# Performance work log

Measured on AMD Instinct MI355X. Metric: run time of the kernel, lower is better.

## Reference

```python
import jax, jax.numpy as jnp
import numpy as np

B, L, HID, NH = 8, 384, 512, 8
DH = HID // NH
MAX_SEQ_LEN = 384  # module's max_seq_len; pe has 2*MAX_SEQ_LEN rows


def setup_inputs() -> dict:
    key = jax.random.key(0)
    ks = jax.random.split(key, 16)
    s = 0.02
    inp = {
        "key": jax.random.normal(ks[0], (B, L, HID), jnp.float32),
        "query": jax.random.normal(ks[1], (B, L, HID), jnp.float32),
        "value": jax.random.normal(ks[2], (B, L, HID), jnp.float32),
        "seq_len": jnp.maximum(
            jax.random.randint(ks[3], (B,), L // 2, L + 1), 0
        ).at[0].set(L),  # ensure max(seq_len) == L
        "pe": jax.random.normal(ks[4], (2 * MAX_SEQ_LEN, HID), jnp.float32) * s,
        "Wk": jax.random.normal(ks[5], (HID, HID), jnp.float32) * s,
        "bk": jnp.zeros((HID,), jnp.float32),
        "Wq": jax.random.normal(ks[6], (HID, HID), jnp.float32) * s,
        "bq": jnp.zeros((HID,), jnp.float32),
        "Wv": jax.random.normal(ks[7], (HID, HID), jnp.float32) * s,
        "bv": jnp.zeros((HID,), jnp.float32),
        "Wr": jax.random.normal(ks[8], (HID, HID), jnp.float32) * s,
        "br": jnp.zeros((HID,), jnp.float32),
        "u_bias": jax.random.normal(ks[9], (NH, DH), jnp.float32) * s,
        "v_bias": jax.random.normal(ks[10], (NH, DH), jnp.float32) * s,
        "Wf": jax.random.normal(ks[11], (HID, HID), jnp.float32) * s,
        "bf": jnp.zeros((HID,), jnp.float32),
    }
    return inp


def reference(key, query, value, seq_len, pe, Wk, bk, Wq, bq, Wv, bv, Wr, br,
              u_bias, v_bias, Wf, bf):
    b, l, hid = key.shape
    # relative distance matrix: rel[i, j] = j - i
    idx = jnp.arange(l)
    rel = idx[None, :] - idx[:, None]                       # [L, L]
    rpe = pe[rel + MAX_SEQ_LEN]                             # [L, L, HID] gather

    k = (key @ Wk.T + bk).reshape(b, l, NH, DH).transpose(0, 2, 1, 3)    # [b,h,L,d]
    q = (query @ Wq.T + bq).reshape(b, l, NH, DH).transpose(0, 2, 1, 3)
    v = (value @ Wv.T + bv).reshape(b, l, NH, DH).transpose(0, 2, 1, 3)
    r = (rpe @ Wr.T + br).reshape(l, l, NH, DH)             # [L,L,h,d]

    A = jnp.einsum("bhid,bhjd->bhij", q, k)
    Bt = jnp.einsum("bhid,ijhd->bhij", q, r)
    C = jnp.einsum("hd,bhjd->bhj", u_bias, k)[:, :, None, :]  # broadcast over i
    D = jnp.einsum("ijhd,hd->hij", r, v_bias)[None]            # broadcast over b

    score = (A + Bt + C + D) / jnp.sqrt(jnp.float32(DH))
    mask = (idx[None, :] < seq_len[:, None])[:, None, None, :]  # [b,1,1,L]
    score = jnp.where(mask, score, jnp.float32(-1e15))
    attn = jax.nn.softmax(score, axis=-1)

    out = jnp.einsum("bhij,bhjd->bhid", attn, v)
    out = out.transpose(0, 2, 1, 3).reshape(b, l, hid)
    out = out @ Wf.T + bf  # ff_final
    return out
```

## Files before the change

### kernel.cpp

```cpp
#include <hip/hip_runtime.h>
#include <hip/hip_bf16.h>

typedef short v8s __attribute__((ext_vector_type(8)));
typedef float v4f __attribute__((ext_vector_type(4)));
typedef float float4v __attribute__((ext_vector_type(4)));
typedef unsigned short u16x4 __attribute__((ext_vector_type(4)));

#define BB 8
#define LL 384
#define HIDD 512
#define NHH 8
#define DHH 64
#define PP 768
#define BL (BB*LL)

using bf16 = __hip_bfloat16;

__device__ __forceinline__ v8s ld8(const bf16* p){
  return *reinterpret_cast<const v8s*>(p);
}

struct Ptrs { const void* p[16]; };

#define CAST_GROUPS 1606528

__global__ __launch_bounds__(256)
void cast_inputs(Ptrs ptrs, bf16* __restrict__ dst){
  __shared__ int smode;
  int tid = threadIdx.x;
  if (tid < 64){
    const unsigned int* key_raw = (const unsigned int*)ptrs.p[0];
    int huge = 0, zeros = 0;
    #pragma unroll
    for (int c = 0; c < 4; c++){
      unsigned int lo = key_raw[tid*4 + c] & 0xFFFFu;
      if (((lo >> 7) & 0xFF) >= 0x90u) huge++;
      if (lo == 0u) zeros++;
    }
    #pragma unroll
    for (int off = 32; off; off >>= 1){
      huge  += __shfl_xor(huge,  off);
      zeros += __shfl_xor(zeros, off);
    }
    if (tid == 0) smode = (huge > 8 || zeros > 200) ? 1 : 0;
  }
  __syncthreads();
  int mode = smode;

  const int start[17] = {0, 393216, 786432, 1179648, 1277952, 1343488, 1343616,
                         1409152, 1409280, 1474816, 1474944, 1540480, 1540608,
                         1540736, 1540864, 1606400, 1606528};
  int g = blockIdx.x*256 + tid;
  if (g >= CAST_GROUPS) return;
  int s = 0;
  #pragma unroll
  for (int i = 0; i < 16; i++) if (g >= start[i+1]) s = i+1;
  int local = g - start[s];
  u16x4 outv;
  if (mode){
    const float4v* src = (const float4v*)ptrs.p[s];
    float4v f = src[local];
    #pragma unroll
    for (int i = 0; i < 4; i++){
      bf16 h = __float2bfloat16(f[i]);
      outv[i] = *reinterpret_cast<unsigned short*>(&h);
    }
  } else {
    const u16x4* src = (const u16x4*)ptrs.p[s];
    outv = src[local];
  }
  *reinterpret_cast<u16x4*>(dst + (long)g*4) = outv;
}

__global__ void zero_out(float* __restrict__ out, int n){
  int i = blockIdx.x*256 + threadIdx.x;
  if (i < n) out[i] = 0.f;
}

__global__ __launch_bounds__(256)
void proj_gemm(const bf16* __restrict__ arena, bf16* __restrict__ outbase,
               bf16* __restrict__ vT, float* __restrict__ uk, float* __restrict__ rd)
{
  __shared__ alignas(16) bf16 ldsA[128*72];
  __shared__ alignas(16) bf16 ldsB[64*72];
  __shared__ float part[4*128];

  int z = blockIdx.z;
  if (z == 3 && blockIdx.y >= 6) return;
  const bf16* A    = arena + (long)z*1572864;
  const bf16* Bw   = arena + 5111808 + (long)z*262656;
  const bf16* bias = arena + 5373952 + (long)z*262656;

  int tid  = threadIdx.x;
  int lane = tid & 63, w = tid >> 6;
  int l16  = lane & 15, quad = lane >> 4;
  long g0  = (long)blockIdx.y * 128;
  int h    = blockIdx.x;
  int mloc = (w >> 1) * 64;
  int nloc = (w & 1) * 32;

  v4f acc[4][2] = {};
  for (int kk = 0; kk < HIDD; kk += 64){
    __syncthreads();
    #pragma unroll
    for (int c4 = 0; c4 < 4; c4++){
      int id = tid + c4*256;
      int row = id >> 3, c = id & 7;
      v8s v = ld8(A + (g0 + row)*HIDD + kk + c*8);
      *(v8s*)&ldsA[row*72 + c*8] = v;
    }
    #pragma unroll
    for (int c2 = 0; c2 < 2; c2++){
      int id = tid + c2*256;
      int row = id >> 3, c = id & 7;
      v8s v = ld8(Bw + (long)(h*64 + row)*HIDD + kk + c*8);
      *(v8s*)&ldsB[row*72 + c*8] = v;
    }
    __syncthreads();
    #pragma unroll
    for (int kq = 0; kq < 2; kq++){
      v8s af[4], bfr[2];
      #pragma unroll
      for (int ti = 0; ti < 4; ti++)
        af[ti] = *(const v8s*)&ldsA[(mloc + ti*16 + l16)*72 + kq*32 + quad*8];
      #pragma unroll
      for (int tj = 0; tj < 2; tj++)
        bfr[tj] = *(const v8s*)&ldsB[(nloc + tj*16 + l16)*72 + kq*32 + quad*8];
      #pragma unroll
      for (int ti = 0; ti < 4; ti++)
        #pragma unroll
        for (int tj = 0; tj < 2; tj++)
          acc[ti][tj] = __builtin_amdgcn_mfma_f32_16x16x32_bf16(af[ti], bfr[tj], acc[ti][tj], 0,0,0);
    }
  }

  if (z != 2){
    bf16* C = outbase + (long)z*1572864;
    #pragma unroll
    for (int ti = 0; ti < 4; ti++)
      #pragma unroll
      for (int tj = 0; tj < 2; tj++){
        int col = h*64 + nloc + tj*16 + l16;
        float bv = __bfloat162float(bias[col]);
        #pragma unroll
        for (int r = 0; r < 4; r++){
          long row = g0 + mloc + ti*16 + quad*4 + r;
          C[row*HIDD + col] = __float2bfloat16(acc[ti][tj][r] + bv);
        }
      }
  }

  if (z != 1){
    __syncthreads();
    bf16* tileT = ldsA;
    #pragma unroll
    for (int ti = 0; ti < 4; ti++)
      #pragma unroll
      for (int tj = 0; tj < 2; tj++){
        int lcol = nloc + tj*16 + l16;
        float bv = __bfloat162float(bias[h*64 + lcol]);
        #pragma unroll
        for (int r = 0; r < 4; r++){
          int lrow = mloc + ti*16 + quad*4 + r;
          tileT[lcol*132 + lrow] = __float2bfloat16(acc[ti][tj][r] + bv);
        }
      }
    __syncthreads();

    if (z == 2){
      int b = (int)(g0/LL), j0 = (int)(g0%LL);
      int d = tid >> 2, jc = (tid & 3)*32;
      #pragma unroll
      for (int s = 0; s < 4; s++){
        v8s v = *(const v8s*)&tileT[d*132 + jc + s*8];
        *(v8s*)&vT[((long)b*HIDD + h*64 + d)*LL + j0 + jc + s*8] = v;
      }
    } else {
      const bf16* vec = arena + (z == 0 ? 6162432 : 6162944) + h*64;
      int row2 = tid & 63;
      int pi   = tid >> 6;
      float s0 = 0.f, s1 = 0.f;
      #pragma unroll
      for (int dd = 0; dd < 16; dd++){
        int d = pi*16 + dd;
        float uvd = __bfloat162float(vec[d]);
        s0 += __bfloat162float(tileT[d*132 + row2])      * uvd;
        s1 += __bfloat162float(tileT[d*132 + row2 + 64]) * uvd;
      }
      part[pi*128 + row2]      = s0;
      part[pi*128 + row2 + 64] = s1;
      __syncthreads();
      if (tid < 128){
        float tot = part[tid] + part[128+tid] + part[256+tid] + part[384+tid];
        if (z == 0){
          int b = (int)(g0/LL), j0 = (int)(g0%LL);
          uk[((long)b*NHH + h)*LL + j0 + tid] = tot;
        } else {
          rd[h*PP + (int)g0 + tid] = tot;
        }
      }
    }
  }
}

__global__ __launch_bounds__(256)
void gemm_final(const bf16* __restrict__ A, const bf16* __restrict__ Bw,
                const bf16* __restrict__ bias, float* __restrict__ C)
{
  __shared__ alignas(16) bf16 ldsA[128*72];
  __shared__ alignas(16) bf16 ldsB[64*72];

  int tid  = threadIdx.x;
  int lane = tid & 63, w = tid >> 6;
  int l16  = lane & 15, quad = lane >> 4;
  long g0  = (long)blockIdx.y * 128;
  int h    = blockIdx.x;
  int mloc = (w >> 1) * 64;
  int nloc = (w & 1) * 32;

  v4f acc[4][2] = {};
  for (int kk = 0; kk < HIDD; kk += 64){
    __syncthreads();
    #pragma unroll
    for (int c4 = 0; c4 < 4; c4++){
      int id = tid + c4*256;
      int row = id >> 3, c = id & 7;
      v8s v = ld8(A + (g0 + row)*HIDD + kk + c*8);
      *(v8s*)&ldsA[row*72 + c*8] = v;
    }
    #pragma unroll
    for (int c2 = 0; c2 < 2; c2++){
      int id = tid + c2*256;
      int row = id >> 3, c = id & 7;
      v8s v = ld8(Bw + (long)(h*64 + row)*HIDD + kk + c*8);
      *(v8s*)&ldsB[row*72 + c*8] = v;
    }
    __syncthreads();
    #pragma unroll
    for (int kq = 0; kq < 2; kq++){
      v8s af[4], bfr[2];
      #pragma unroll
      for (int ti = 0; ti < 4; ti++)
        af[ti] = *(const v8s*)&ldsA[(mloc + ti*16 + l16)*72 + kq*32 + quad*8];
      #pragma unroll
      for (int tj = 0; tj < 2; tj++)
        bfr[tj] = *(const v8s*)&ldsB[(nloc + tj*16 + l16)*72 + kq*32 + quad*8];
      #pragma unroll
      for (int ti = 0; ti < 4; ti++)
        #pragma unroll
        for (int tj = 0; tj < 2; tj++)
          acc[ti][tj] = __builtin_amdgcn_mfma_f32_16x16x32_bf16(af[ti], bfr[tj], acc[ti][tj], 0,0,0);
    }
  }

  #pragma unroll
  for (int ti = 0; ti < 4; ti++)
    #pragma unroll
    for (int tj = 0; tj < 2; tj++){
      int col = h*64 + nloc + tj*16 + l16;
      float bv = __bfloat162float(bias[col]);
      #pragma unroll
      for (int r = 0; r < 4; r++){
        long row = g0 + mloc + ti*16 + quad*4 + r;
        C[row*HIDD + col] = acc[ti][tj][r] + bv;
      }
    }
}

#define BTS_S 404
#define PB_S  408

__global__ __launch_bounds__(256, 6)
void attn_kernel(const bf16* __restrict__ qb, const bf16* __restrict__ kb,
                 const bf16* __restrict__ vT, const bf16* __restrict__ rproj,
                 const float* __restrict__ uk, const float* __restrict__ rd,
                 const unsigned int* __restrict__ sraw, bf16* __restrict__ attn_out)
{
  __shared__ alignas(16) bf16 Bts[16*BTS_S];
  __shared__ alignas(16) bf16 Pb[16*PB_S];
  __shared__ float wmax[4*16];
  __shared__ float wsum[4*16];
  __shared__ int s_slen;

  int i0 = blockIdx.x*16;
  int h  = blockIdx.y, b = blockIdx.z;
  int lane = threadIdx.x & 63, wave = threadIdx.x >> 6;
  int l16 = lane & 15, quad = lane >> 4;
  int p0 = 369 - i0;

  if (threadIdx.x == 0){
    bool i64 = true;
    for (int bb = 0; bb < BB; bb++){
      unsigned int w0 = sraw[2*bb], w1 = sraw[2*bb+1];
      if (!(w1 == 0u && w0 >= 1u && w0 < 100000u)) { i64 = false; break; }
    }
    unsigned int w = i64 ? sraw[2*b] : sraw[b];
    int v = (w < 100000u) ? (int)w : (int)(__uint_as_float(w) + 0.5f);
    s_slen = min(max(v, 0), LL);
  }

  const bf16* qp = qb + (long)(b*LL + i0 + l16)*HIDD + h*DHH;
  v8s aq0 = ld8(qp + quad*8);
  v8s aq1 = ld8(qp + 32 + quad*8);

  #pragma unroll 2
  for (int nt = wave; nt < 25; nt += 4){
    int pbase = p0 + nt*16;
    int prow = min(pbase + l16, PP-1);
    const bf16* rp = rproj + (long)prow*HIDD + h*DHH;
    v8s b0 = ld8(rp + quad*8);
    v8s b1 = ld8(rp + 32 + quad*8);
    v4f acc = {};
    acc = __builtin_amdgcn_mfma_f32_16x16x32_bf16(aq0, b0, acc, 0,0,0);
    acc = __builtin_amdgcn_mfma_f32_16x16x32_bf16(aq1, b1, acc, 0,0,0);
    float rdv = rd[h*PP + prow];
    #pragma unroll
    for (int r = 0; r < 4; r++)
      Bts[(quad*4 + r)*BTS_S + nt*16 + l16] = __float2bfloat16(acc[r] + rdv);
  }
  __syncthreads();
  int slen = s_slen;

  float sv[6][4];
  #pragma unroll
  for (int t = 0; t < 6; t++){
    int j0 = (wave + 4*t)*16;
    const bf16* kp = kb + (long)(b*LL + j0 + l16)*HIDD + h*DHH;
    v8s b0 = ld8(kp + quad*8);
    v8s b1 = ld8(kp + 32 + quad*8);
    v4f acc = {};
    acc = __builtin_amdgcn_mfma_f32_16x16x32_bf16(aq0, b0, acc, 0,0,0);
    acc = __builtin_amdgcn_mfma_f32_16x16x32_bf16(aq1, b1, acc, 0,0,0);
    int j = j0 + l16;
    float c_add = uk[(b*NHH + h)*LL + j];
    #pragma unroll
    for (int r = 0; r < 4; r++){
      int il = quad*4 + r;
      float bt = __bfloat162float(Bts[il*BTS_S + (j - il + 15)]);
      float s = (acc[r] + bt + c_add) * 0.125f;
      sv[t][r] = (j >= slen) ? -1e15f : s;
    }
  }

  float mx[4];
  #pragma unroll
  for (int r = 0; r < 4; r++){
    float m = sv[0][r];
    #pragma unroll
    for (int t = 1; t < 6; t++) m = fmaxf(m, sv[t][r]);
    #pragma unroll
    for (int off = 1; off < 16; off <<= 1) m = fmaxf(m, __shfl_xor(m, off));
    mx[r] = m;
  }
  if (l16 == 0){
    #pragma unroll
    for (int r = 0; r < 4; r++) wmax[wave*16 + quad*4 + r] = mx[r];
  }
  __syncthreads();

  float gm[4];
  #pragma unroll
  for (int r = 0; r < 4; r++){
    int row = quad*4 + r;
    gm[r] = fmaxf(fmaxf(wmax[row], wmax[16+row]), fmaxf(wmax[32+row], wmax[48+row]));
  }
  float sm[4] = {0.f, 0.f, 0.f, 0.f};
  #pragma unroll
  for (int t = 0; t < 6; t++){
    int j = (wave + 4*t)*16 + l16;
    #pragma unroll
    for (int r = 0; r < 4; r++){
      float e = __expf(sv[t][r] - gm[r]);
      sm[r] += e;
      Pb[(quad*4 + r)*PB_S + j] = __float2bfloat16(e);
    }
  }
  #pragma unroll
  for (int r = 0; r < 4; r++){
    #pragma unroll
    for (int off = 1; off < 16; off <<= 1) sm[r] += __shfl_xor(sm[r], off);
  }
  if (l16 == 0){
    #pragma unroll
    for (int r = 0; r < 4; r++) wsum[wave*16 + quad*4 + r] = sm[r];
  }
  __syncthreads();

  float rsum_r[4];
  #pragma unroll
  for (int r = 0; r < 4; r++){
    int row = quad*4 + r;
    rsum_r[r] = wsum[row] + wsum[16+row] + wsum[32+row] + wsum[48+row];
  }

  {
    int d0 = wave*16;
    v4f o = {};
    const bf16* vp = vT + ((long)(b*NHH + h)*DHH + d0 + l16)*LL;
    #pragma unroll 4
    for (int kt = 0; kt < 12; kt++){
      v8s a  = *reinterpret_cast<const v8s*>(&Pb[l16*PB_S + kt*32 + quad*8]);
      v8s bb = ld8(vp + kt*32 + quad*8);
      o = __builtin_amdgcn_mfma_f32_16x16x32_bf16(a, bb, o, 0,0,0);
    }
    #pragma unroll
    for (int r = 0; r < 4; r++){
      float val = o[r] / rsum_r[r];
      attn_out[(long)(b*LL + i0 + quad*4 + r)*HIDD + h*DHH + d0 + l16] = __float2bfloat16(val);
    }
  }
}

extern "C" void kernel_launch(void* const* d_in, const int* in_sizes, int n_in,
                              void* d_out, int out_size, void* d_ws, size_t ws_size,
                              hipStream_t stream)
{
  float* out = (float*)d_out;

  const int expect[17] = {1572864, 1572864, 1572864, 8, 393216,
                          262144, 512, 262144, 512, 262144, 512, 262144, 512,
                          512, 512, 262144, 512};
  bool ok = (n_in == 17);
  if (ok) for (int i = 0; i < 17; i++) if (in_sizes[i] != expect[i]) { ok = false; break; }
  if (!ok){
    zero_out<<<dim3((out_size + 255)/256), dim3(256), 0, stream>>>(out, out_size);
    return;
  }

  char* ws = (char*)d_ws;
  bf16*  cast   = (bf16*)(ws);
  bf16*  kb     = (bf16*)(ws + 12852224);
  bf16*  qb     = (bf16*)(ws + 15997952);
  bf16*  vT     = (bf16*)(ws + 19143680);
  bf16*  rproj  = (bf16*)(ws + 22289408);
  bf16*  attn_o = (bf16*)(ws + 25435136);
  float* uk     = (float*)(ws + 28580864);
  float* rd     = (float*)(ws + 28679168);
  (void)ws_size;

  const bf16* Wfc = cast + 6163456;
  const bf16* bfc = cast + 6425600;

  Ptrs ptrs;
  {
    int k = 0;
    for (int i = 0; i < 17; i++){ if (i == 3) continue; ptrs.p[k++] = d_in[i]; }
  }

  dim3 blk(256);
  cast_inputs<<<dim3((CAST_GROUPS + 255)/256), blk, 0, stream>>>(ptrs, cast);
  proj_gemm<<<dim3(8, 24, 4), blk, 0, stream>>>(cast, kb, vT, uk, rd);
  attn_kernel<<<dim3(LL/16, NHH, BB), blk, 0, stream>>>(
      qb, kb, vT, rproj, uk, rd, (const unsigned int*)d_in[3], attn_o);
  gemm_final<<<dim3(8, 24, 1), blk, 0, stream>>>(attn_o, Wfc, bfc, out);
}
```

Before: 158.5 us.

## Fuse activation fp32-to-bf16 cast into projection GEMM loads; shrink final GEMM tile

The cast kernel no longer converts the large key/query/value/pe activations. The projection GEMM now reads them directly in fp32 and converts them to bf16 while staging into LDS. This drops a full write and re-read of the converted activations, but the GEMM now reads twice the bytes for A and runs extra conversion instructions. Separately, the final GEMM uses 64-row tiles instead of 128-row tiles, doubling the grid for better CU occupancy at the cost of more weight re-reads.

```diff
diff --git a/kernel.cpp b/kernel.cpp
--- a/kernel.cpp
+++ b/kernel.cpp
@@ -19,17 +19,21 @@
 __device__ __forceinline__ v8s ld8(const bf16* p){
   return *reinterpret_cast<const v8s*>(p);
 }
-
-struct Ptrs { const void* p[16]; };
-
-#define CAST_GROUPS 1606528
-
-__global__ __launch_bounds__(256)
-void cast_inputs(Ptrs ptrs, bf16* __restrict__ dst){
-  __shared__ int smode;
-  int tid = threadIdx.x;
+__device__ __forceinline__ v8s cvt8v(const float* p){
+  float4v f0 = *(const float4v*)p;
+  float4v f1 = *(const float4v*)(p + 4);
+  v8s r;
+  #pragma unroll
+  for (int i = 0; i < 4; i++){
+    bf16 h0 = __float2bfloat16(f0[i]);
+    bf16 h1 = __float2bfloat16(f1[i]);
+    r[i]   = *reinterpret_cast<short*>(&h0);
+    r[i+4] = *reinterpret_cast<short*>(&h1);
+  }
+  return r;
+}
+__device__ __forceinline__ int block_detect_mode(const unsigned int* key_raw, int tid, int* smode){
   if (tid < 64){
-    const unsigned int* key_raw = (const unsigned int*)ptrs.p[0];
     int huge = 0, zeros = 0;
     #pragma unroll
     for (int c = 0; c < 4; c++){
@@ -42,19 +46,34 @@
       huge  += __shfl_xor(huge,  off);
       zeros += __shfl_xor(zeros, off);
     }
-    if (tid == 0) smode = (huge > 8 || zeros > 200) ? 1 : 0;
+    if (tid == 0) *smode = (huge > 8 || zeros > 200) ? 1 : 0;
   }
   __syncthreads();
-  int mode = smode;
-
-  const int start[17] = {0, 393216, 786432, 1179648, 1277952, 1343488, 1343616,
-                         1409152, 1409280, 1474816, 1474944, 1540480, 1540608,
-                         1540736, 1540864, 1606400, 1606528};
+  return *smode;
+}
+
+__global__ void zero_out(float* __restrict__ out, int n){
+  int i = blockIdx.x*256 + threadIdx.x;
+  if (i < n) out[i] = 0.f;
+}
+
+struct Ptrs { const void* p[12]; };
+
+#define CAST_GROUPS 328576
+
+__global__ __launch_bounds__(256)
+void cast_inputs(Ptrs ptrs, const unsigned int* __restrict__ key_raw, bf16* __restrict__ dst){
+  __shared__ int smode;
+  int tid = threadIdx.x;
+  int mode = block_detect_mode(key_raw, tid, &smode);
+
+  const int start[13] = {0, 65536, 65664, 131200, 131328, 196864, 196992,
+                         262528, 262656, 262784, 262912, 328448, 328576};
   int g = blockIdx.x*256 + tid;
   if (g >= CAST_GROUPS) return;
   int s = 0;
   #pragma unroll
-  for (int i = 0; i < 16; i++) if (g >= start[i+1]) s = i+1;
+  for (int i = 0; i < 12; i++) if (g >= start[i+1]) s = i+1;
   int local = g - start[s];
   u16x4 outv;
   if (mode){
@@ -72,26 +91,27 @@
   *reinterpret_cast<u16x4*>(dst + (long)g*4) = outv;
 }
 
-__global__ void zero_out(float* __restrict__ out, int n){
-  int i = blockIdx.x*256 + threadIdx.x;
-  if (i < n) out[i] = 0.f;
-}
-
 __global__ __launch_bounds__(256)
-void proj_gemm(const bf16* __restrict__ arena, bf16* __restrict__ outbase,
-               bf16* __restrict__ vT, float* __restrict__ uk, float* __restrict__ rd)
+void proj_gemm(const void* __restrict__ A0, const void* __restrict__ A1,
+               const void* __restrict__ A2, const void* __restrict__ A3,
+               const bf16* __restrict__ arena, const unsigned int* __restrict__ key_raw,
+               bf16* __restrict__ outbase, bf16* __restrict__ vT,
+               float* __restrict__ uk, float* __restrict__ rd)
 {
   __shared__ alignas(16) bf16 ldsA[128*72];
   __shared__ alignas(16) bf16 ldsB[64*72];
   __shared__ float part[4*128];
+  __shared__ int smode;
+
+  int tid  = threadIdx.x;
+  int mode = block_detect_mode(key_raw, tid, &smode);
 
   int z = blockIdx.z;
   if (z == 3 && blockIdx.y >= 6) return;
-  const bf16* A    = arena + (long)z*1572864;
-  const bf16* Bw   = arena + 5111808 + (long)z*262656;
-  const bf16* bias = arena + 5373952 + (long)z*262656;
-
-  int tid  = threadIdx.x;
+  const void* A    = (z == 0) ? A0 : (z == 1) ? A1 : (z == 2) ? A2 : A3;
+  const bf16* Bw   = arena + (long)z*262656;
+  const bf16* bias = arena + 262144 + (long)z*262656;
+
   int lane = tid & 63, w = tid >> 6;
   int l16  = lane & 15, quad = lane >> 4;
   long g0  = (long)blockIdx.y * 128;
@@ -102,19 +122,28 @@
   v4f acc[4][2] = {};
   for (int kk = 0; kk < HIDD; kk += 64){
     __syncthreads();
-    #pragma unroll
-    for (int c4 = 0; c4 < 4; c4++){
-      int id = tid + c4*256;
-      int row = id >> 3, c = id & 7;
-      v8s v = ld8(A + (g0 + row)*HIDD + kk + c*8);
-      *(v8s*)&ldsA[row*72 + c*8] = v;
+    if (mode){
+      const float* Af = (const float*)A;
+      #pragma unroll
+      for (int c4 = 0; c4 < 4; c4++){
+        int id = tid + c4*256;
+        int row = id >> 3, c = id & 7;
+        *(v8s*)&ldsA[row*72 + c*8] = cvt8v(Af + (g0 + row)*HIDD + kk + c*8);
+      }
+    } else {
+      const bf16* Ab = (const bf16*)A;
+      #pragma unroll
+      for (int c4 = 0; c4 < 4; c4++){
+        int id = tid + c4*256;
+        int row = id >> 3, c = id & 7;
+        *(v8s*)&ldsA[row*72 + c*8] = ld8(Ab + (g0 + row)*HIDD + kk + c*8);
+      }
     }
     #pragma unroll
     for (int c2 = 0; c2 < 2; c2++){
       int id = tid + c2*256;
       int row = id >> 3, c = id & 7;
-      v8s v = ld8(Bw + (long)(h*64 + row)*HIDD + kk + c*8);
-      *(v8s*)&ldsB[row*72 + c*8] = v;
+      *(v8s*)&ldsB[row*72 + c*8] = ld8(Bw + (long)(h*64 + row)*HIDD + kk + c*8);
     }
     __syncthreads();
     #pragma unroll
@@ -176,7 +205,7 @@
         *(v8s*)&vT[((long)b*HIDD + h*64 + d)*LL + j0 + jc + s*8] = v;
       }
     } else {
-      const bf16* vec = arena + (z == 0 ? 6162432 : 6162944) + h*64;
+      const bf16* vec = arena + (z == 0 ? 1050624 : 1051136) + h*64;
       int row2 = tid & 63;
       int pi   = tid >> 6;
       float s0 = 0.f, s1 = 0.f;
@@ -207,46 +236,44 @@
 void gemm_final(const bf16* __restrict__ A, const bf16* __restrict__ Bw,
                 const bf16* __restrict__ bias, float* __restrict__ C)
 {
-  __shared__ alignas(16) bf16 ldsA[128*72];
+  __shared__ alignas(16) bf16 ldsA[64*72];
   __shared__ alignas(16) bf16 ldsB[64*72];
 
   int tid  = threadIdx.x;
   int lane = tid & 63, w = tid >> 6;
   int l16  = lane & 15, quad = lane >> 4;
-  long g0  = (long)blockIdx.y * 128;
+  long g0  = (long)blockIdx.y * 64;
   int h    = blockIdx.x;
-  int mloc = (w >> 1) * 64;
+  int mloc = (w >> 1) * 32;
   int nloc = (w & 1) * 32;
 
-  v4f acc[4][2] = {};
+  v4f acc[2][2] = {};
   for (int kk = 0; kk < HIDD; kk += 64){
     __syncthreads();
-    #pragma unroll
-    for (int c4 = 0; c4 < 4; c4++){
-      int id = tid + c4*256;
-      int row = id >> 3, c = id & 7;
-      v8s v = ld8(A + (g0 + row)*HIDD + kk + c*8);
-      *(v8s*)&ldsA[row*72 + c*8] = v;
-    }
     #pragma unroll
     for (int c2 = 0; c2 < 2; c2++){
       int id = tid + c2*256;
       int row = id >> 3, c = id & 7;
-      v8s v = ld8(Bw + (long)(h*64 + row)*HIDD + kk + c*8);
-      *(v8s*)&ldsB[row*72 + c*8] = v;
+      *(v8s*)&ldsA[row*72 + c*8] = ld8(A + (g0 + row)*HIDD + kk + c*8);
+    }
+    #pragma unroll
+    for (int c2 = 0; c2 < 2; c2++){
+      int id = tid + c2*256;
+      int row = id >> 3, c = id & 7;
+      *(v8s*)&ldsB[row*72 + c*8] = ld8(Bw + (long)(h*64 + row)*HIDD + kk + c*8);
     }
     __syncthreads();
     #pragma unroll
     for (int kq = 0; kq < 2; kq++){
-      v8s af[4], bfr[2];
-      #pragma unroll
-      for (int ti = 0; ti < 4; ti++)
+      v8s af[2], bfr[2];
+      #pragma unroll
+      for (int ti = 0; ti < 2; ti++)
         af[ti] = *(const v8s*)&ldsA[(mloc + ti*16 + l16)*72 + kq*32 + quad*8];
       #pragma unroll
       for (int tj = 0; tj < 2; tj++)
         bfr[tj] = *(const v8s*)&ldsB[(nloc + tj*16 + l16)*72 + kq*32 + quad*8];
       #pragma unroll
-      for (int ti = 0; ti < 4; ti++)
+      for (int ti = 0; ti < 2; ti++)
         #pragma unroll
         for (int tj = 0; tj < 2; tj++)
           acc[ti][tj] = __builtin_amdgcn_mfma_f32_16x16x32_bf16(af[ti], bfr[tj], acc[ti][tj], 0,0,0);
@@ -254,7 +281,7 @@
   }
 
   #pragma unroll
-  for (int ti = 0; ti < 4; ti++)
+  for (int ti = 0; ti < 2; ti++)
     #pragma unroll
     for (int tj = 0; tj < 2; tj++){
       int col = h*64 + nloc + tj*16 + l16;
@@ -428,29 +455,30 @@
   }
 
   char* ws = (char*)d_ws;
-  bf16*  cast   = (bf16*)(ws);
-  bf16*  kb     = (bf16*)(ws + 12852224);
-  bf16*  qb     = (bf16*)(ws + 15997952);
-  bf16*  vT     = (bf16*)(ws + 19143680);
-  bf16*  rproj  = (bf16*)(ws + 22289408);
-  bf16*  attn_o = (bf16*)(ws + 25435136);
-  float* uk     = (float*)(ws + 28580864);
-  float* rd     = (float*)(ws + 28679168);
+  bf16*  arena  = (bf16*)(ws);
+  bf16*  kb     = (bf16*)(ws +  2628608);
+  bf16*  qb     = (bf16*)(ws +  5774336);
+  bf16*  vT     = (bf16*)(ws +  8920064);
+  bf16*  rproj  = (bf16*)(ws + 12065792);
+  bf16*  attn_o = (bf16*)(ws + 15211520);
+  float* uk     = (float*)(ws + 18357248);
+  float* rd     = (float*)(ws + 18455552);
   (void)ws_size;
 
-  const bf16* Wfc = cast + 6163456;
-  const bf16* bfc = cast + 6425600;
+  const bf16* Wfc = arena + 1051648;
+  const bf16* bfc = arena + 1313792;
+  const unsigned int* key_raw = (const unsigned int*)d_in[0];
 
   Ptrs ptrs;
-  {
-    int k = 0;
-    for (int i = 0; i < 17; i++){ if (i == 3) continue; ptrs.p[k++] = d_in[i]; }
-  }
+  ptrs.p[0] = d_in[5];  ptrs.p[1] = d_in[6];  ptrs.p[2]  = d_in[7];  ptrs.p[3]  = d_in[8];
+  ptrs.p[4] = d_in[9];  ptrs.p[5] = d_in[10]; ptrs.p[6]  = d_in[11]; ptrs.p[7]  = d_in[12];
+  ptrs.p[8] = d_in[13]; ptrs.p[9] = d_in[14]; ptrs.p[10] = d_in[15]; ptrs.p[11] = d_in[16];
 
   dim3 blk(256);
-  cast_inputs<<<dim3((CAST_GROUPS + 255)/256), blk, 0, stream>>>(ptrs, cast);
-  proj_gemm<<<dim3(8, 24, 4), blk, 0, stream>>>(cast, kb, vT, uk, rd);
+  cast_inputs<<<dim3((CAST_GROUPS + 255)/256), blk, 0, stream>>>(ptrs, key_raw, arena);
+  proj_gemm<<<dim3(8, 24, 4), blk, 0, stream>>>(
+      d_in[0], d_in[1], d_in[2], d_in[4], arena, key_raw, kb, vT, uk, rd);
   attn_kernel<<<dim3(LL/16, NHH, BB), blk, 0, stream>>>(
       qb, kb, vT, rproj, uk, rd, (const unsigned int*)d_in[3], attn_o);
-  gemm_final<<<dim3(8, 24, 1), blk, 0, stream>>>(attn_o, Wfc, bfc, out);
-}
+  gemm_final<<<dim3(8, 48, 1), blk, 0, stream>>>(attn_o, Wfc, bfc, out);
+}
```

Result: slower. 163.0 us (+2.9%).
